# Kernel tuning notes

Hardware: AMD Instinct MI355X
Metric: run time of the kernel (lower is better)

Reference implementation:

```python
import jax, jax.numpy as jnp
import numpy as np

BN_EPS = 1e-5


def _square_distance(src, dst):
    # src: (B,N,3), dst: (B,S,3) -> (B,N,S) squared euclidean distance
    d = -2.0 * jnp.einsum('bnc,bsc->bns', src, dst)
    d += jnp.sum(src * src, -1)[:, :, None]
    d += jnp.sum(dst * dst, -1)[:, None, :]
    return d


def _bn_relu(x, gamma, beta):
    # training-mode BatchNorm1d over (B, C, N): stats over (B, N)
    mean = jnp.mean(x, axis=(0, 2), keepdims=True)
    var = jnp.var(x, axis=(0, 2), keepdims=True)  # biased, as torch uses for normalization
    xhat = (x - mean) * jax.lax.rsqrt(var + BN_EPS)
    return jax.nn.relu(xhat * gamma[None, :, None] + beta[None, :, None])


def setup_inputs() -> dict:
    key = jax.random.key(0)
    ks = jax.random.split(key, 8)
    B, N, S, C1, C2 = 4, 8192, 2048, 128, 256
    inp = {
        'xyz1': jax.random.normal(ks[0], (B, 3, N), jnp.float32),
        'xyz2': jax.random.normal(ks[1], (B, 3, S), jnp.float32),
        'points1': jax.random.normal(ks[2], (B, C1, N), jnp.float32),
        'points2': jax.random.normal(ks[3], (B, C2, S), jnp.float32),
        'w0': jax.random.normal(ks[4], (256, C1 + C2), jnp.float32) * (1.0 / np.sqrt(C1 + C2)),
        'b0': jnp.zeros((256,), jnp.float32),
        'gamma0': jnp.ones((256,), jnp.float32),
        'beta0': jnp.zeros((256,), jnp.float32),
        'w1': jax.random.normal(ks[5], (128, 256), jnp.float32) * (1.0 / np.sqrt(256)),
        'b1': jnp.zeros((128,), jnp.float32),
        'gamma1': jnp.ones((128,), jnp.float32),
        'beta1': jnp.zeros((128,), jnp.float32),
    }
    return inp


def reference(xyz1, xyz2, points1, points2, w0, b0, gamma0, beta0, w1, b1, gamma1, beta1):
    B, _, N = xyz1.shape
    S = xyz2.shape[2]
    xyz1_t = jnp.transpose(xyz1, (0, 2, 1))  # (B,N,3)
    xyz2_t = jnp.transpose(xyz2, (0, 2, 1))  # (B,S,3)
    dist = _square_distance(xyz1_t, xyz2_t)  # (B,N,S)
    neg_d3, idx = jax.lax.top_k(-dist, 3)    # 3 smallest distances
    d3 = -neg_d3                             # (B,N,3)
    dist_recip = 1.0 / (d3 + 1e-8)
    weight = dist_recip / jnp.sum(dist_recip, axis=2, keepdims=True)  # (B,N,3)
    points2_t = jnp.transpose(points2, (0, 2, 1))  # (B,S,C2)
    bidx = jnp.arange(B)[:, None, None]
    neighbor = points2_t[bidx, idx]                 # (B,N,3,C2)
    interp = jnp.sum(neighbor * weight[..., None], axis=2)  # (B,N,C2)
    interp = jnp.transpose(interp, (0, 2, 1))               # (B,C2,N)
    x = jnp.concatenate([points1, interp], axis=1)          # (B,C1+C2,N)
    x = _bn_relu(jnp.einsum('oc,bcn->bon', w0, x) + b0[None, :, None], gamma0, beta0)
    x = _bn_relu(jnp.einsum('oc,bcn->bon', w1, x) + b1[None, :, None], gamma1, beta1)
    return x
```

## Files before the change

kernel.cpp:

```cpp
#include <hip/hip_runtime.h>
#include <hip/hip_bf16.h>

#define BATCH 4
#define NPTS  8192
#define SPTS  2048
#define C1    128
#define C2    256
#define CIN   384
#define H0    256
#define H1    128

typedef __attribute__((ext_vector_type(8))) short bf16x8;
typedef __attribute__((ext_vector_type(4))) float f32x4;

__device__ __forceinline__ unsigned short f2bf(float x) {
  union { float f; unsigned u; } v; v.f = x;
  unsigned r = v.u + 0x7fff + ((v.u >> 16) & 1);
  return (unsigned short)(r >> 16);
}
__device__ __forceinline__ float bf2f(unsigned short u) {
  union { unsigned u; float f; } v; v.u = ((unsigned)u) << 16; return v.f;
}

__global__ __launch_bounds__(256) void prep_kernel(
    const float* __restrict__ p2, unsigned short* __restrict__ p2tb,
    const float* __restrict__ xyz2, float4* __restrict__ xp,
    const float* __restrict__ w0, const float* __restrict__ w1,
    unsigned short* __restrict__ Wp,
    const float* __restrict__ p1, unsigned short* __restrict__ Xp) {
  __shared__ unsigned short shmem[64 * 136];
  int bid = blockIdx.x;
  int t = threadIdx.x;

  if (bid < 512) {
    int b = bid >> 7, rem = bid & 127;
    int s0 = (rem >> 2) * 64, c0 = (rem & 3) * 64;
    const float* src = p2 + (size_t)b * C2 * SPTS;
    int ss = t & 63, cseg = t >> 6;
#pragma unroll
    for (int i = 0; i < 16; i++) {
      int cc = cseg + i * 4;
      shmem[ss * 72 + cc] = f2bf(src[(size_t)(c0 + cc) * SPTS + s0 + ss]);
    }
    __syncthreads();
    int s = t >> 2, chunk = t & 3;
    uint4 v0 = *(const uint4*)&shmem[s * 72 + chunk * 16];
    uint4 v1 = *(const uint4*)&shmem[s * 72 + chunk * 16 + 8];
    unsigned short* dst = p2tb + (size_t)b * SPTS * C2 + (size_t)(s0 + s) * C2 + c0 + chunk * 16;
    *(uint4*)dst = v0;
    *(uint4*)(dst + 8) = v1;
  } else if (bid < 1024) {
    int b2 = bid - 512;
    int b = b2 >> 7, n0 = (b2 & 127) * 64;
    int nn = t & 63, c4 = t >> 6;
#pragma unroll
    for (int i = 0; i < 32; i++) {
      int c = i * 4 + c4;
      shmem[nn * 136 + c] = f2bf(p1[((size_t)b * C1 + c) * NPTS + n0 + nn]);
    }
    __syncthreads();
    int n = t >> 2;
#pragma unroll
    for (int j = 0; j < 4; j++) {
      int ch = (t & 3) + j * 4;
      uint4 v = *(const uint4*)&shmem[n * 136 + ch * 8];
      *(uint4*)&Xp[((size_t)b * NPTS + n0 + n) * CIN + ch * 8] = v;
    }
  } else if (bid < 1056) {
    int idx = (bid - 1024) * 256 + t;
    int b = idx >> 11, s = idx & (SPTS - 1);
    const float* x2 = xyz2 + (size_t)b * 3 * SPTS;
    float x = x2[s], y = x2[SPTS + s], z = x2[2 * SPTS + s];
    xp[idx] = make_float4(x, y, z, x * x + y * y + z * z);
  } else {
    int idx = ((bid - 1056) * 256 + t) * 4;
    const float* src = (idx < H0 * CIN) ? (w0 + idx) : (w1 + (idx - H0 * CIN));
    float4 v = *(const float4*)src;
    ushort4 o;
    o.x = f2bf(v.x); o.y = f2bf(v.y); o.z = f2bf(v.z); o.w = f2bf(v.w);
    *(ushort4*)(Wp + idx) = o;
  }
}

#define INS3(d, s, e0, e1, e2, j0, j1, j2)                        \
  {                                                               \
    bool lt0 = (d) < (e0), lt1 = (d) < (e1), lt2 = (d) < (e2);    \
    j2 = lt1 ? (j1) : (lt2 ? (s) : (j2));                         \
    j1 = lt0 ? (j0) : (lt1 ? (s) : (j1));                         \
    j0 = lt0 ? (s) : (j0);                                        \
    e2 = __builtin_amdgcn_fmed3f((d), (e1), (e2));                \
    e1 = __builtin_amdgcn_fmed3f((d), (e0), (e1));                \
    e0 = fminf((d), (e0));                                        \
  }

__global__ __launch_bounds__(1024) void knn_kernel(
    const float* __restrict__ xyz1, const float4* __restrict__ xp,
    int* __restrict__ nidx, float* __restrict__ nw) {
  int b = blockIdx.y;
  int t = threadIdx.x;
  int lane = t & 63;
  int w = __builtin_amdgcn_readfirstlane(t >> 6);
  int n = blockIdx.x * 64 + lane;
  const float* x1 = xyz1 + (size_t)b * 3 * NPTS;
  float px = x1[n], py = x1[NPTS + n], pz = x1[2 * NPTS + n];

  const int CHUNK = SPTS / 16;
  int sbase = w * CHUNK;
  const float4* cp = xp + (size_t)b * SPTS + sbase;

  float d0 = 3e38f, d1 = 3e38f, d2 = 3e38f;
  int i0 = 0, i1 = 0, i2 = 0;
#pragma unroll 8
  for (int j = 0; j < CHUNK; j++) {
    float4 c = cp[j];
    float qc = fmaf(py, c.y, px * c.x);
    qc = fmaf(pz, c.z, qc);
    float d = fmaf(-2.f, qc, c.w);
    int s = sbase + j;
    INS3(d, s, d0, d1, d2, i0, i1, i2);
  }

  __shared__ float dsh[16][64][3];
  __shared__ int   ish[16][64][3];
  dsh[w][lane][0] = d0; dsh[w][lane][1] = d1; dsh[w][lane][2] = d2;
  ish[w][lane][0] = i0; ish[w][lane][1] = i1; ish[w][lane][2] = i2;
  __syncthreads();

  if (t < 256) {
    int g = t >> 6, q = t & 63;
    float e0 = 3e38f, e1 = 3e38f, e2 = 3e38f;
    int j0 = 0, j1 = 0, j2 = 0;
#pragma unroll
    for (int c = 0; c < 4; c++) {
#pragma unroll
      for (int k = 0; k < 3; k++) {
        float d = dsh[4 * g + c][q][k];
        int s = ish[4 * g + c][q][k];
        INS3(d, s, e0, e1, e2, j0, j1, j2);
      }
    }
    dsh[4 * g][q][0] = e0; dsh[4 * g][q][1] = e1; dsh[4 * g][q][2] = e2;
    ish[4 * g][q][0] = j0; ish[4 * g][q][1] = j1; ish[4 * g][q][2] = j2;
  }
  __syncthreads();

  if (t < 64) {
    float e0 = 3e38f, e1 = 3e38f, e2 = 3e38f;
    int j0 = 0, j1 = 0, j2 = 0;
#pragma unroll
    for (int c = 0; c < 4; c++) {
#pragma unroll
      for (int k = 0; k < 3; k++) {
        float d = dsh[4 * c][t][k];
        int s = ish[4 * c][t][k];
        INS3(d, s, e0, e1, e2, j0, j1, j2);
      }
    }
    float qq = px * px + py * py + pz * pz;
    float r0 = 1.f / (e0 + qq + 1e-8f);
    float r1 = 1.f / (e1 + qq + 1e-8f);
    float r2 = 1.f / (e2 + qq + 1e-8f);
    float rs = 1.f / (r0 + r1 + r2);
    int base = (b * NPTS + n) * 3;
    nidx[base + 0] = j0; nidx[base + 1] = j1; nidx[base + 2] = j2;
    nw[base + 0] = r0 * rs; nw[base + 1] = r1 * rs; nw[base + 2] = r2 * rs;
  }
}

__global__ __launch_bounds__(256) void interp_kernel(
    const unsigned short* __restrict__ p2tb, const int* __restrict__ nidx,
    const float* __restrict__ nw, unsigned short* __restrict__ Xp) {
  const int PTS = 8;
  int bid = blockIdx.x;
  int b = bid / (NPTS / PTS);
  int p0 = (bid % (NPTS / PTS)) * PTS;
  int c = threadIdx.x;
  const unsigned short* base = p2tb + (size_t)b * SPTS * C2;
#pragma unroll
  for (int k = 0; k < PTS; k++) {
    int p = p0 + k;
    int ib = (b * NPTS + p) * 3;
    int i0 = nidx[ib], i1 = nidx[ib + 1], i2 = nidx[ib + 2];
    float w0v = nw[ib], w1v = nw[ib + 1], w2v = nw[ib + 2];
    float v = w0v * bf2f(base[(size_t)i0 * C2 + c]) +
              w1v * bf2f(base[(size_t)i1 * C2 + c]) +
              w2v * bf2f(base[(size_t)i2 * C2 + c]);
    Xp[((size_t)b * NPTS + p) * CIN + C1 + c] = f2bf(v);
  }
}

template <int MT, int KD, bool OUT_BF16>
__global__ __launch_bounds__(256) void mfma_gemm_kernel(
    const unsigned short* __restrict__ A, const unsigned short* __restrict__ X,
    const float* __restrict__ bias, void* __restrict__ Yv) {
  __shared__ unsigned short As[128 * 32];
  __shared__ unsigned short Bs[128 * 32];
  int b = blockIdx.z;
  int n0 = blockIdx.x * 128;
  int o0 = blockIdx.y * 128;
  int t = threadIdx.x;
  int lane = t & 63;
  int w = __builtin_amdgcn_readfirstlane(t >> 6);
  int mhalf = (w & 1) * 64, nhalf = (w >> 1) * 64;
  const unsigned short* Xb = X + (size_t)b * NPTS * KD;

  f32x4 acc[4][4] = {};

  int rA = lane >> 2;
  int cofs = (lane & 3) * 8;

  for (int k0 = 0; k0 < KD; k0 += 32) {
#pragma unroll
    for (int q = 0; q < 2; q++) {
      int r0 = w * 32 + q * 16;
      const unsigned short* ga = A + (size_t)(o0 + r0 + rA) * KD + k0 + cofs;
      __builtin_amdgcn_global_load_lds(
          (const __attribute__((address_space(1))) void*)ga,
          (__attribute__((address_space(3))) void*)(As + r0 * 32), 16, 0, 0);
      const unsigned short* gb = Xb + (size_t)(n0 + r0 + rA) * KD + k0 + cofs;
      __builtin_amdgcn_global_load_lds(
          (const __attribute__((address_space(1))) void*)gb,
          (__attribute__((address_space(3))) void*)(Bs + r0 * 32), 16, 0, 0);
    }
    __syncthreads();

    bf16x8 af[4], bfr[4];
    int mi = lane & 15, kq = (lane >> 4) * 8;
#pragma unroll
    for (int i = 0; i < 4; i++) {
      af[i]  = *(const bf16x8*)(As + (mhalf + i * 16 + mi) * 32 + kq);
      bfr[i] = *(const bf16x8*)(Bs + (nhalf + i * 16 + mi) * 32 + kq);
    }
#pragma unroll
    for (int mt = 0; mt < 4; mt++)
#pragma unroll
      for (int nt = 0; nt < 4; nt++)
        acc[mt][nt] = __builtin_amdgcn_mfma_f32_16x16x32_bf16(
            af[mt], bfr[nt], acc[mt][nt], 0, 0, 0);
    __syncthreads();
  }

  int mi = lane & 15;
  int rq = (lane >> 4) * 4;
#pragma unroll
  for (int mt = 0; mt < 4; mt++) {
#pragma unroll
    for (int r = 0; r < 4; r++) {
      int m = o0 + mhalf + mt * 16 + rq + r;
      float bv = bias[m];
#pragma unroll
      for (int nt = 0; nt < 4; nt++) {
        int n = n0 + nhalf + nt * 16 + mi;
        float v = acc[mt][nt][r] + bv;
        if constexpr (OUT_BF16) {
          unsigned short* Y = (unsigned short*)Yv + (size_t)b * MT * NPTS;
          Y[(size_t)m * NPTS + n] = f2bf(v);
        } else {
          float* Y = (float*)Yv + (size_t)b * MT * NPTS;
          Y[(size_t)m * NPTS + n] = v;
        }
      }
    }
  }
}

template <int C>
__global__ __launch_bounds__(256) void bn_stats_bf16_kernel(
    const unsigned short* __restrict__ Y, const float* __restrict__ gamma,
    const float* __restrict__ beta, float* __restrict__ a, float* __restrict__ s) {
  int o = blockIdx.x;
  int t = threadIdx.x;
  float sum = 0.f, sq = 0.f;
  for (int b = 0; b < BATCH; b++) {
    const unsigned short* p = Y + ((size_t)b * C + o) * NPTS;
    for (int n = t * 4; n < NPTS; n += 1024) {
      ushort4 v = *(const ushort4*)(p + n);
      float x0 = bf2f(v.x), x1 = bf2f(v.y), x2 = bf2f(v.z), x3 = bf2f(v.w);
      sum += x0 + x1 + x2 + x3;
      sq += x0 * x0 + x1 * x1 + x2 * x2 + x3 * x3;
    }
  }
  __shared__ float r1[256], r2[256];
  r1[t] = sum; r2[t] = sq;
  __syncthreads();
  for (int off = 128; off > 0; off >>= 1) {
    if (t < off) { r1[t] += r1[t + off]; r2[t] += r2[t + off]; }
    __syncthreads();
  }
  if (t == 0) {
    float inv = 1.f / (float)(BATCH * NPTS);
    float mean = r1[0] * inv;
    float var = r2[0] * inv - mean * mean;
    float ia = gamma[o] * rsqrtf(var + 1e-5f);
    a[o] = ia;
    s[o] = beta[o] - mean * ia;
  }
}

template <int C>
__global__ __launch_bounds__(256) void bn_stats_kernel(
    const float* __restrict__ Y, const float* __restrict__ gamma,
    const float* __restrict__ beta, float* __restrict__ a, float* __restrict__ s) {
  int o = blockIdx.x;
  int t = threadIdx.x;
  float sum = 0.f, sq = 0.f;
  for (int b = 0; b < BATCH; b++) {
    const float* p = Y + ((size_t)b * C + o) * NPTS;
    for (int n = t * 4; n < NPTS; n += 1024) {
      float4 v = *(const float4*)(p + n);
      sum += v.x + v.y + v.z + v.w;
      sq += v.x * v.x + v.y * v.y + v.z * v.z + v.w * v.w;
    }
  }
  __shared__ float r1[256], r2[256];
  r1[t] = sum; r2[t] = sq;
  __syncthreads();
  for (int off = 128; off > 0; off >>= 1) {
    if (t < off) { r1[t] += r1[t + off]; r2[t] += r2[t + off]; }
    __syncthreads();
  }
  if (t == 0) {
    float inv = 1.f / (float)(BATCH * NPTS);
    float mean = r1[0] * inv;
    float var = r2[0] * inv - mean * mean;
    float ia = gamma[o] * rsqrtf(var + 1e-5f);
    a[o] = ia;
    s[o] = beta[o] - mean * ia;
  }
}

__global__ __launch_bounds__(256) void bn0_apply_kernel(
    const unsigned short* __restrict__ Y0, const float* __restrict__ a,
    const float* __restrict__ s, unsigned short* __restrict__ X1) {
  __shared__ unsigned short tile[64][80];
  int b = blockIdx.z, o0 = blockIdx.y * 64, n0 = blockIdx.x * 64;
  int t = threadIdx.x;
  int nn = t & 63, o4 = t >> 6;
#pragma unroll
  for (int i = 0; i < 16; i++) {
    int o = i * 4 + o4;
    float v = bf2f(Y0[((size_t)b * H0 + o0 + o) * NPTS + n0 + nn]);
    v = fmaxf(v * a[o0 + o] + s[o0 + o], 0.f);
    tile[nn][o] = f2bf(v);
  }
  __syncthreads();
  int n = t >> 2;
#pragma unroll
  for (int j = 0; j < 2; j++) {
    int ch = (t & 3) + j * 4;
    uint4 v = *(const uint4*)&tile[n][ch * 8];
    *(uint4*)&X1[((size_t)b * NPTS + n0 + n) * H0 + o0 + ch * 8] = v;
  }
}

__global__ __launch_bounds__(256) void bn_apply_kernel(
    float* __restrict__ Y, const float* __restrict__ a, const float* __restrict__ s) {
  int idx = blockIdx.x * 256 + threadIdx.x;
  int i = idx * 4;
  int c = (i >> 13) & (H1 - 1);
  float ia = a[c], sh = s[c];
  float4 v = *(float4*)(Y + i);
  v.x = fmaxf(v.x * ia + sh, 0.f);
  v.y = fmaxf(v.y * ia + sh, 0.f);
  v.z = fmaxf(v.z * ia + sh, 0.f);
  v.w = fmaxf(v.w * ia + sh, 0.f);
  *(float4*)(Y + i) = v;
}

extern "C" void kernel_launch(void* const* d_in, const int* in_sizes, int n_in,
                              void* d_out, int out_size, void* d_ws, size_t ws_size,
                              hipStream_t stream) {
  const float* xyz1    = (const float*)d_in[0];
  const float* xyz2    = (const float*)d_in[1];
  const float* points1 = (const float*)d_in[2];
  const float* points2 = (const float*)d_in[3];
  const float* w0      = (const float*)d_in[4];
  const float* b0      = (const float*)d_in[5];
  const float* gamma0  = (const float*)d_in[6];
  const float* beta0   = (const float*)d_in[7];
  const float* w1      = (const float*)d_in[8];
  const float* b1      = (const float*)d_in[9];
  const float* gamma1  = (const float*)d_in[10];
  const float* beta1   = (const float*)d_in[11];
  float* out = (float*)d_out;

  char* ws = (char*)d_ws;
  unsigned short* p2tb = (unsigned short*)ws;  ws += (size_t)BATCH * SPTS * C2 * 2;
  unsigned short* Xp = (unsigned short*)ws;    ws += (size_t)BATCH * NPTS * CIN * 2;
  unsigned short* Y0 = (unsigned short*)ws;    ws += (size_t)BATCH * H0 * NPTS * 2;
  unsigned short* X1 = (unsigned short*)ws;    ws += (size_t)BATCH * NPTS * H0 * 2;
  unsigned short* Wp = (unsigned short*)ws;    ws += (size_t)(H0 * CIN + H1 * H0) * 2;
  int* nidx = (int*)ws;                        ws += (size_t)BATCH * NPTS * 3 * 4;
  float* nw = (float*)ws;                      ws += (size_t)BATCH * NPTS * 3 * 4;
  float4* xyz2p = (float4*)(((uintptr_t)ws + 15) & ~(uintptr_t)15);
  ws = (char*)xyz2p + (size_t)BATCH * SPTS * 16;
  float* a0 = (float*)ws;                      ws += 1024;
  float* s0 = (float*)ws;                      ws += 1024;
  float* a1 = (float*)ws;                      ws += 1024;
  float* s1 = (float*)ws;                      ws += 1024;
  (void)ws_size; (void)in_sizes; (void)n_in; (void)out_size;

  prep_kernel<<<dim3(1184), 256, 0, stream>>>(points2, p2tb, xyz2, xyz2p,
                                              w0, w1, Wp, points1, Xp);
  knn_kernel<<<dim3(NPTS / 64, BATCH), 1024, 0, stream>>>(xyz1, xyz2p, nidx, nw);
  interp_kernel<<<dim3(BATCH * NPTS / 8), 256, 0, stream>>>(p2tb, nidx, nw, Xp);

  mfma_gemm_kernel<H0, CIN, true><<<dim3(NPTS / 128, H0 / 128, BATCH), 256, 0, stream>>>(
      Wp, Xp, b0, Y0);
  bn_stats_bf16_kernel<H0><<<H0, 256, 0, stream>>>(Y0, gamma0, beta0, a0, s0);
  bn0_apply_kernel<<<dim3(NPTS / 64, H0 / 64, BATCH), 256, 0, stream>>>(Y0, a0, s0, X1);
  mfma_gemm_kernel<H1, H0, false><<<dim3(NPTS / 128, H1 / 128, BATCH), 256, 0, stream>>>(
      Wp + H0 * CIN, X1, b1, out);
  bn_stats_kernel<H1><<<H1, 256, 0, stream>>>(out, gamma1, beta1, a1, s1);
  bn_apply_kernel<<<dim3(BATCH * H1 * NPTS / 1024), 256, 0, stream>>>(out, a1, s1);
}
```

Before: 196.6 us.

## Fuse BatchNorm statistics into GEMM epilogues via atomic accumulation

Removes the two separate BN statistics kernels. Each GEMM epilogue now computes per-channel partial sums and sums of squares, reduces them across 16 lanes with shuffles, and accumulates them into global buffers with atomicAdd. The apply kernels derive scale and shift from those sums. The buffers are zeroed by an extra block in the prep kernel. This drops two full re-reads of the intermediate activations and two launches, in exchange for atomic contention and a nondeterministic summation order. Layer 0 statistics are now taken from fp32 values before the bf16 rounding, not from the stored bf16 outputs.

```diff
diff --git a/kernel.cpp b/kernel.cpp
--- a/kernel.cpp
+++ b/kernel.cpp
@@ -27,7 +27,8 @@
     const float* __restrict__ xyz2, float4* __restrict__ xp,
     const float* __restrict__ w0, const float* __restrict__ w1,
     unsigned short* __restrict__ Wp,
-    const float* __restrict__ p1, unsigned short* __restrict__ Xp) {
+    const float* __restrict__ p1, unsigned short* __restrict__ Xp,
+    float* __restrict__ stats) {
   __shared__ unsigned short shmem[64 * 136];
   int bid = blockIdx.x;
   int t = threadIdx.x;
@@ -72,13 +73,15 @@
     const float* x2 = xyz2 + (size_t)b * 3 * SPTS;
     float x = x2[s], y = x2[SPTS + s], z = x2[2 * SPTS + s];
     xp[idx] = make_float4(x, y, z, x * x + y * y + z * z);
-  } else {
+  } else if (bid < 1184) {
     int idx = ((bid - 1056) * 256 + t) * 4;
     const float* src = (idx < H0 * CIN) ? (w0 + idx) : (w1 + (idx - H0 * CIN));
     float4 v = *(const float4*)src;
     ushort4 o;
     o.x = f2bf(v.x); o.y = f2bf(v.y); o.z = f2bf(v.z); o.w = f2bf(v.w);
     *(ushort4*)(Wp + idx) = o;
+  } else {
+    for (int i = t; i < 768; i += 256) stats[i] = 0.f;
   }
 }
 
@@ -192,7 +195,8 @@
 template <int MT, int KD, bool OUT_BF16>
 __global__ __launch_bounds__(256) void mfma_gemm_kernel(
     const unsigned short* __restrict__ A, const unsigned short* __restrict__ X,
-    const float* __restrict__ bias, void* __restrict__ Yv) {
+    const float* __restrict__ bias, void* __restrict__ Yv,
+    float* __restrict__ sumb, float* __restrict__ sqb) {
   __shared__ unsigned short As[128 * 32];
   __shared__ unsigned short Bs[128 * 32];
   int b = blockIdx.z;
@@ -248,10 +252,12 @@
     for (int r = 0; r < 4; r++) {
       int m = o0 + mhalf + mt * 16 + rq + r;
       float bv = bias[m];
+      float ps = 0.f, pq = 0.f;
 #pragma unroll
       for (int nt = 0; nt < 4; nt++) {
         int n = n0 + nhalf + nt * 16 + mi;
         float v = acc[mt][nt][r] + bv;
+        ps += v; pq += v * v;
         if constexpr (OUT_BF16) {
           unsigned short* Y = (unsigned short*)Yv + (size_t)b * MT * NPTS;
           Y[(size_t)m * NPTS + n] = f2bf(v);
@@ -260,87 +266,41 @@
           Y[(size_t)m * NPTS + n] = v;
         }
       }
-    }
-  }
-}
-
-template <int C>
-__global__ __launch_bounds__(256) void bn_stats_bf16_kernel(
-    const unsigned short* __restrict__ Y, const float* __restrict__ gamma,
-    const float* __restrict__ beta, float* __restrict__ a, float* __restrict__ s) {
-  int o = blockIdx.x;
-  int t = threadIdx.x;
-  float sum = 0.f, sq = 0.f;
-  for (int b = 0; b < BATCH; b++) {
-    const unsigned short* p = Y + ((size_t)b * C + o) * NPTS;
-    for (int n = t * 4; n < NPTS; n += 1024) {
-      ushort4 v = *(const ushort4*)(p + n);
-      float x0 = bf2f(v.x), x1 = bf2f(v.y), x2 = bf2f(v.z), x3 = bf2f(v.w);
-      sum += x0 + x1 + x2 + x3;
-      sq += x0 * x0 + x1 * x1 + x2 * x2 + x3 * x3;
-    }
-  }
-  __shared__ float r1[256], r2[256];
-  r1[t] = sum; r2[t] = sq;
-  __syncthreads();
-  for (int off = 128; off > 0; off >>= 1) {
-    if (t < off) { r1[t] += r1[t + off]; r2[t] += r2[t + off]; }
-    __syncthreads();
-  }
-  if (t == 0) {
-    float inv = 1.f / (float)(BATCH * NPTS);
-    float mean = r1[0] * inv;
-    float var = r2[0] * inv - mean * mean;
-    float ia = gamma[o] * rsqrtf(var + 1e-5f);
-    a[o] = ia;
-    s[o] = beta[o] - mean * ia;
-  }
-}
-
-template <int C>
-__global__ __launch_bounds__(256) void bn_stats_kernel(
-    const float* __restrict__ Y, const float* __restrict__ gamma,
-    const float* __restrict__ beta, float* __restrict__ a, float* __restrict__ s) {
-  int o = blockIdx.x;
-  int t = threadIdx.x;
-  float sum = 0.f, sq = 0.f;
-  for (int b = 0; b < BATCH; b++) {
-    const float* p = Y + ((size_t)b * C + o) * NPTS;
-    for (int n = t * 4; n < NPTS; n += 1024) {
-      float4 v = *(const float4*)(p + n);
-      sum += v.x + v.y + v.z + v.w;
-      sq += v.x * v.x + v.y * v.y + v.z * v.z + v.w * v.w;
-    }
-  }
-  __shared__ float r1[256], r2[256];
-  r1[t] = sum; r2[t] = sq;
-  __syncthreads();
-  for (int off = 128; off > 0; off >>= 1) {
-    if (t < off) { r1[t] += r1[t + off]; r2[t] += r2[t + off]; }
-    __syncthreads();
-  }
-  if (t == 0) {
-    float inv = 1.f / (float)(BATCH * NPTS);
-    float mean = r1[0] * inv;
-    float var = r2[0] * inv - mean * mean;
-    float ia = gamma[o] * rsqrtf(var + 1e-5f);
-    a[o] = ia;
-    s[o] = beta[o] - mean * ia;
+#pragma unroll
+      for (int off = 1; off < 16; off <<= 1) {
+        ps += __shfl_xor(ps, off, 16);
+        pq += __shfl_xor(pq, off, 16);
+      }
+      if (mi == 0) {
+        atomicAdd(&sumb[m], ps);
+        atomicAdd(&sqb[m], pq);
+      }
+    }
   }
 }
 
 __global__ __launch_bounds__(256) void bn0_apply_kernel(
-    const unsigned short* __restrict__ Y0, const float* __restrict__ a,
-    const float* __restrict__ s, unsigned short* __restrict__ X1) {
+    const unsigned short* __restrict__ Y0, const float* __restrict__ sumb,
+    const float* __restrict__ sqb, const float* __restrict__ gamma,
+    const float* __restrict__ beta, unsigned short* __restrict__ X1) {
   __shared__ unsigned short tile[64][80];
+  __shared__ float aS[64], sS[64];
   int b = blockIdx.z, o0 = blockIdx.y * 64, n0 = blockIdx.x * 64;
   int t = threadIdx.x;
+  if (t < 64) {
+    const float inv = 1.f / (float)(BATCH * NPTS);
+    float mean = sumb[o0 + t] * inv;
+    float var = sqb[o0 + t] * inv - mean * mean;
+    float ia = gamma[o0 + t] * rsqrtf(var + 1e-5f);
+    aS[t] = ia; sS[t] = beta[o0 + t] - mean * ia;
+  }
+  __syncthreads();
   int nn = t & 63, o4 = t >> 6;
 #pragma unroll
   for (int i = 0; i < 16; i++) {
     int o = i * 4 + o4;
     float v = bf2f(Y0[((size_t)b * H0 + o0 + o) * NPTS + n0 + nn]);
-    v = fmaxf(v * a[o0 + o] + s[o0 + o], 0.f);
+    v = fmaxf(v * aS[o] + sS[o], 0.f);
     tile[nn][o] = f2bf(v);
   }
   __syncthreads();
@@ -354,11 +314,22 @@
 }
 
 __global__ __launch_bounds__(256) void bn_apply_kernel(
-    float* __restrict__ Y, const float* __restrict__ a, const float* __restrict__ s) {
-  int idx = blockIdx.x * 256 + threadIdx.x;
-  int i = idx * 4;
-  int c = (i >> 13) & (H1 - 1);
-  float ia = a[c], sh = s[c];
+    float* __restrict__ Y, const float* __restrict__ sumb,
+    const float* __restrict__ sqb, const float* __restrict__ gamma,
+    const float* __restrict__ beta) {
+  __shared__ float sh2[2];
+  int idx0 = blockIdx.x * 1024;
+  int c = (idx0 >> 13) & (H1 - 1);
+  if (threadIdx.x == 0) {
+    const float inv = 1.f / (float)(BATCH * NPTS);
+    float mean = sumb[c] * inv;
+    float var = sqb[c] * inv - mean * mean;
+    float ia = gamma[c] * rsqrtf(var + 1e-5f);
+    sh2[0] = ia; sh2[1] = beta[c] - mean * ia;
+  }
+  __syncthreads();
+  float ia = sh2[0], sh = sh2[1];
+  int i = idx0 + threadIdx.x * 4;
   float4 v = *(float4*)(Y + i);
   v.x = fmaxf(v.x * ia + sh, 0.f);
   v.y = fmaxf(v.y * ia + sh, 0.f);
@@ -394,23 +365,24 @@
   float* nw = (float*)ws;                      ws += (size_t)BATCH * NPTS * 3 * 4;
   float4* xyz2p = (float4*)(((uintptr_t)ws + 15) & ~(uintptr_t)15);
   ws = (char*)xyz2p + (size_t)BATCH * SPTS * 16;
-  float* a0 = (float*)ws;                      ws += 1024;
-  float* s0 = (float*)ws;                      ws += 1024;
-  float* a1 = (float*)ws;                      ws += 1024;
-  float* s1 = (float*)ws;                      ws += 1024;
+  float* stats = (float*)ws;                   ws += 4096;
+  float* sum0 = stats;
+  float* sq0  = stats + 256;
+  float* sum1 = stats + 512;
+  float* sq1  = stats + 640;
   (void)ws_size; (void)in_sizes; (void)n_in; (void)out_size;
 
-  prep_kernel<<<dim3(1184), 256, 0, stream>>>(points2, p2tb, xyz2, xyz2p,
-                                              w0, w1, Wp, points1, Xp);
+  prep_kernel<<<dim3(1185), 256, 0, stream>>>(points2, p2tb, xyz2, xyz2p,
+                                              w0, w1, Wp, points1, Xp, stats);
   knn_kernel<<<dim3(NPTS / 64, BATCH), 1024, 0, stream>>>(xyz1, xyz2p, nidx, nw);
   interp_kernel<<<dim3(BATCH * NPTS / 8), 256, 0, stream>>>(p2tb, nidx, nw, Xp);
 
   mfma_gemm_kernel<H0, CIN, true><<<dim3(NPTS / 128, H0 / 128, BATCH), 256, 0, stream>>>(
-      Wp, Xp, b0, Y0);
-  bn_stats_bf16_kernel<H0><<<H0, 256, 0, stream>>>(Y0, gamma0, beta0, a0, s0);
-  bn0_apply_kernel<<<dim3(NPTS / 64, H0 / 64, BATCH), 256, 0, stream>>>(Y0, a0, s0, X1);
+      Wp, Xp, b0, Y0, sum0, sq0);
+  bn0_apply_kernel<<<dim3(NPTS / 64, H0 / 64, BATCH), 256, 0, stream>>>(
+      Y0, sum0, sq0, gamma0, beta0, X1);
   mfma_gemm_kernel<H1, H0, false><<<dim3(NPTS / 128, H1 / 128, BATCH), 256, 0, stream>>>(
-      Wp + H0 * CIN, X1, b1, out);
-  bn_stats_kernel<H1><<<H1, 256, 0, stream>>>(out, gamma1, beta1, a1, s1);
-  bn_apply_kernel<<<dim3(BATCH * H1 * NPTS / 1024), 256, 0, stream>>>(out, a1, s1);
-}
+      Wp + H0 * CIN, X1, b1, out, sum1, sq1);
+  bn_apply_kernel<<<dim3(BATCH * H1 * NPTS / 1024), 256, 0, stream>>>(
+      out, sum1, sq1, gamma1, beta1);
+}
```

Measured after the change: 316.0 us. 60.8% more time.
